# Kernel tuning notes

Measured on AMD Instinct MI355X. Metric: run time of the kernel, lower is better.

## Reference

```python
import jax, jax.numpy as jnp
import numpy as np

B, T, IN, H, OUT = 1024, 2048, 16, 128, 1


def setup_inputs() -> dict:
    key = jax.random.key(0)
    ks = jax.random.split(key, 4)
    x = jax.random.normal(ks[0], (B, T, IN), dtype=jnp.float32)
    W_ih = jax.random.normal(ks[1], (4 * H, IN), dtype=jnp.float32) * (1.0 / np.sqrt(H))
    W_hh = jax.random.normal(ks[2], (4 * H, H), dtype=jnp.float32) * (1.0 / np.sqrt(H))
    b_ih = jnp.zeros((4 * H,), dtype=jnp.float32)
    b_hh = jnp.zeros((4 * H,), dtype=jnp.float32)
    # xavier_normal_ for fc.weight, zeros for bias
    fc_w = jax.random.normal(ks[3], (OUT, H), dtype=jnp.float32) * np.sqrt(2.0 / (H + OUT))
    fc_b = jnp.zeros((OUT,), dtype=jnp.float32)
    return {"x": x, "W_ih": W_ih, "W_hh": W_hh, "b_ih": b_ih,
            "b_hh": b_hh, "fc_w": fc_w, "fc_b": fc_b}


def reference(x, W_ih, W_hh, b_ih, b_hh, fc_w, fc_b):
    # SLSTM with reset_mechanism='none': mem == LSTM hidden h, syn == cell c;
    # spikes are discarded, so this is a plain LSTMCell recurrence + final Linear.
    b, t, _ = x.shape
    h = W_hh.shape[1]
    # Precompute input contribution to gates for all timesteps: (T, B, 4H)
    xg = jnp.einsum('bti,gi->tbg', x, W_ih) + (b_ih + b_hh)

    def step(carry, xg_t):
        h_t, c_t = carry
        gates = xg_t + h_t @ W_hh.T  # (B, 4H)
        i_g, f_g, g_g, o_g = jnp.split(gates, 4, axis=-1)
        c_new = jax.nn.sigmoid(f_g) * c_t + jax.nn.sigmoid(i_g) * jnp.tanh(g_g)
        h_new = jax.nn.sigmoid(o_g) * jnp.tanh(c_new)
        return (h_new, c_new), None

    h0 = jnp.zeros((b, h), dtype=x.dtype)
    c0 = jnp.zeros((b, h), dtype=x.dtype)
    (h_final, _), _ = jax.lax.scan(step, (h0, c0), xg)
    return h_final @ fc_w.T + fc_b  # fc(mem)
```

## Files before the change

### kernel.cpp

```cpp
#include <hip/hip_runtime.h>
#include <hip/hip_bf16.h>


#define T_LEN 2048
#define IN_DIM 16
#define CHUNK 32
#define NROWS 4

typedef __attribute__((ext_vector_type(4))) float f32x4;
typedef __attribute__((ext_vector_type(8))) short s16x8;

__device__ __forceinline__ short f2bf(float f) {
    union { float f; unsigned u; } v; v.f = f;
    unsigned r = v.u + 0x7fffu + ((v.u >> 16) & 1u);
    return (short)(r >> 16);
}
__device__ __forceinline__ unsigned pk_bf16(float a, float b) {
#if __has_builtin(__builtin_amdgcn_cvt_pk_bf16_f32)
    typedef __attribute__((ext_vector_type(2))) __bf16 bf16x2;
    bf16x2 r = __builtin_amdgcn_cvt_pk_bf16_f32(a, b);
    union { bf16x2 v; unsigned u; } c; c.v = r;
    return c.u;
#else
    return (unsigned)(unsigned short)f2bf(a) | ((unsigned)(unsigned short)f2bf(b) << 16);
#endif
}
__device__ __forceinline__ float pack4(float r0, float r1, float r2, float r3) {
    int d = __float_as_int(r0);
    d = __builtin_amdgcn_update_dpp(d, __float_as_int(r1), 0x124, 0xF, 0x2, false);
    d = __builtin_amdgcn_update_dpp(d, __float_as_int(r2), 0x128, 0xF, 0x4, false);
    d = __builtin_amdgcn_update_dpp(d, __float_as_int(r3), 0x12C, 0xF, 0x8, false);
    return __int_as_float(d);
}

__global__ __launch_bounds__(512, 2)
void slstm_persistent(const float* __restrict__ x,
                      const float* __restrict__ W_ih,
                      const float* __restrict__ W_hh,
                      const float* __restrict__ b_ih,
                      const float* __restrict__ b_hh,
                      const float* __restrict__ fc_w,
                      const float* __restrict__ fc_b,
                      float* __restrict__ out)
{
    __shared__ __align__(16) unsigned short h_frag[2][512];
    __shared__ __align__(16) unsigned short xlds[2][CHUNK][2][4][8];
    __shared__ float red[NROWS];

    const int tid  = threadIdx.x;
    const int lane = tid & 63;
    const int wv   = tid >> 6;
    const int c16  = lane & 15;
    const int quad = lane >> 4;
    const int b0   = blockIdx.x * NROWS;

    const float kNL2E = -1.44269504f;

    s16x8 wfrag[4][5];
    f32x4 biasC[4];
    #pragma unroll
    for (int g = 0; g < 4; ++g) {
        const float scale = (g == 2) ? (2.0f * kNL2E) : kNL2E;
        const int n = g * 128 + wv * 16 + c16;
        #pragma unroll
        for (int kf = 0; kf < 5; ++kf) {
            s16x8 fr;
            #pragma unroll
            for (int j = 0; j < 8; ++j) {
                const int k = kf * 32 + quad * 8 + j;
                float v;
                if (kf < 4) v = W_hh[n * 128 + k];
                else {
                    const int kk = k - 128;
                    v = (kk < IN_DIM) ? W_ih[n * IN_DIM + kk] : 0.0f;
                }
                fr[j] = f2bf(v * scale);
            }
            wfrag[g][kf] = fr;
        }
        #pragma unroll
        for (int r = 0; r < 4; ++r) {
            const int m = g * 128 + wv * 16 + quad * 4 + r;
            biasC[g][r] = (b_ih[m] + b_hh[m]) * scale;
        }
    }

    if (tid < 256) ((unsigned*)h_frag)[tid] = 0;

    const int e    = c16 >> 2;
    const int nb   = c16 & 3;
    const int col  = wv * 16 + quad * 4 + e;
    const int waddr = (col >> 5) * 128 + ((col >> 3) & 3) * 32 + nb * 8 + (col & 7);
    const int hoff = (c16 < 4) ? ((quad * 4 + c16) * 16) : 0;
    const bool xv = (quad < 2) && (c16 < 4);
    const int xoff  = xv ? (quad * 64 + c16 * 16) : 0;
    const int xmask = xv ? ~0 : 0;

    float c_st = 0.0f, h_ep = 0.0f;

    f32x4 xreg;
    {
        const int flat4 = tid * 4;
        const int b_loc = flat4 >> 9;
        const int rem   = flat4 & 511;
        const float* xr = x + (size_t)(b0 + b_loc) * (T_LEN * IN_DIM);
        f32x4 v4 = *(const f32x4*)(xr + rem);
        const int slot = rem >> 4, feat = rem & 15;
        unsigned* dst = (unsigned*)&xlds[0][slot][feat >> 3][b_loc][feat & 7];
        dst[0] = pk_bf16(v4[0], v4[1]);
        dst[1] = pk_bf16(v4[2], v4[3]);
        xreg = *(const f32x4*)(xr + CHUNK * IN_DIM + rem);
    }
    __syncthreads();

    f32x4 accA[4], accB[4];
    {
        s16x8 zx0 = *(const s16x8*)((const char*)xlds + (xoff & xmask));
        #pragma unroll
        for (int g = 0; g < 4; ++g)
            accA[g] = __builtin_amdgcn_mfma_f32_16x16x32_bf16(wfrag[g][4], zx0, biasC[g], 0, 0, 0);
    }

    int off_cur = 128 + xoff;

    auto step_impl = [&](const int RB, const int WB, f32x4 (&aci)[4], f32x4 (&aco)[4]) {
        const char* hb = (const char*)h_frag[RB];
        s16x8 zf[4];
        #pragma unroll
        for (int kf = 0; kf < 4; ++kf)
            zf[kf] = *(const s16x8*)(hb + hoff + kf * 256);
        s16x8 zxn = *(const s16x8*)((const char*)xlds + (off_cur & xmask));
        off_cur = (off_cur + 128) & 8191;

        #pragma unroll
        for (int kf = 0; kf < 4; ++kf) {
            aci[2] = __builtin_amdgcn_mfma_f32_16x16x32_bf16(wfrag[2][kf], zf[kf], aci[2], 0, 0, 0);
            aci[0] = __builtin_amdgcn_mfma_f32_16x16x32_bf16(wfrag[0][kf], zf[kf], aci[0], 0, 0, 0);
            aci[1] = __builtin_amdgcn_mfma_f32_16x16x32_bf16(wfrag[1][kf], zf[kf], aci[1], 0, 0, 0);
        }
        __builtin_amdgcn_sched_barrier(0);

        aci[3] = __builtin_amdgcn_mfma_f32_16x16x32_bf16(wfrag[3][0], zf[0], aci[3], 0, 0, 0);
        aci[3] = __builtin_amdgcn_mfma_f32_16x16x32_bf16(wfrag[3][1], zf[1], aci[3], 0, 0, 0);
        aci[3] = __builtin_amdgcn_mfma_f32_16x16x32_bf16(wfrag[3][2], zf[2], aci[3], 0, 0, 0);
        aci[3] = __builtin_amdgcn_mfma_f32_16x16x32_bf16(wfrag[3][3], zf[3], aci[3], 0, 0, 0);
        const float dg = pack4(aci[2][0], aci[2][1], aci[2][2], aci[2][3]);
        const float eg = __builtin_amdgcn_exp2f(dg);
        const float di = pack4(aci[0][0], aci[0][1], aci[0][2], aci[0][3]);
        const float ei = __builtin_amdgcn_exp2f(di);
        const float df = pack4(aci[1][0], aci[1][1], aci[1][2], aci[1][3]);
        const float ef = __builtin_amdgcn_exp2f(df);
        const float af  = 1.0f + ef;
        const float t1  = (1.0f + ei) * (1.0f + eg);
        const float num = fmaf(c_st, t1, (1.0f - eg) * af);
        const float den = af * t1;
        const float dojj = pack4(aci[3][0], aci[3][1], aci[3][2], aci[3][3]);
        const float eo  = __builtin_amdgcn_exp2f(dojj);
        const float p_o = 1.0f + eo;
        #pragma unroll
        for (int kq = 0; kq < 4; ++kq) {
            __builtin_amdgcn_sched_group_barrier(0x008, 1, 0);
            __builtin_amdgcn_sched_group_barrier(0x002, 6, 0);
        }
        __builtin_amdgcn_sched_barrier(0);

        aco[0] = __builtin_amdgcn_mfma_f32_16x16x32_bf16(wfrag[0][4], zxn, biasC[0], 0, 0, 0);
        aco[1] = __builtin_amdgcn_mfma_f32_16x16x32_bf16(wfrag[1][4], zxn, biasC[1], 0, 0, 0);
        const float cn = num * __builtin_amdgcn_rcpf(den);
        c_st = cn;
        const float ec = __builtin_amdgcn_exp2f(fminf(cn * (2.0f * kNL2E), 40.f));
        const float hn = (1.0f - ec) * __builtin_amdgcn_rcpf(p_o * (1.0f + ec));
        h_ep = hn;
        h_frag[WB][waddr] = (unsigned short)pk_bf16(hn, hn);
        aco[2] = __builtin_amdgcn_mfma_f32_16x16x32_bf16(wfrag[2][4], zxn, biasC[2], 0, 0, 0);
        aco[3] = __builtin_amdgcn_mfma_f32_16x16x32_bf16(wfrag[3][4], zxn, biasC[3], 0, 0, 0);
        __syncthreads();
    };

    for (int t = 0; t < T_LEN; t += 2) {
        step_impl(0, 1, accA, accB);

        const int iter  = (t >> 1) & 15;
        const int cbase = t & ~(CHUNK - 1);
        if (iter < 2) {
            if (cbase + CHUNK < T_LEN) {
                const int flat4 = tid * 4;
                const int b_loc = flat4 >> 9;
                const int rem   = flat4 & 511;
                const int slot = rem >> 4, feat = rem & 15;
                const int nb1 = ((cbase >> 5) + 1) & 1;
                unsigned* dst = (unsigned*)&xlds[nb1][slot][feat >> 3][b_loc][(feat & 7) + 2 * iter];
                dst[0] = pk_bf16(xreg[2 * iter], xreg[2 * iter + 1]);
            }
        } else if (iter == 8) {
            const int tnext = cbase + 2 * CHUNK;
            if (tnext < T_LEN) {
                const int flat4 = tid * 4;
                const int b_loc = flat4 >> 9;
                const int rem   = flat4 & 511;
                xreg = *(const f32x4*)(x + (size_t)(b0 + b_loc) * (T_LEN * IN_DIM)
                                         + (size_t)tnext * IN_DIM + rem);
            }
        }

        step_impl(1, 0, accB, accA);
    }

    float v = h_ep * fc_w[col];
    v += __shfl_xor(v, 4);
    v += __shfl_xor(v, 8);
    v += __shfl_xor(v, 16);
    v += __shfl_xor(v, 32);
    if (tid < NROWS) red[tid] = 0.0f;
    __syncthreads();
    if (lane < NROWS) atomicAdd(&red[nb], v);
    __syncthreads();
    if (tid < NROWS) out[b0 + tid] = red[tid] + fc_b[0];
}

extern "C" void kernel_launch(void* const* d_in, const int* in_sizes, int n_in,
                              void* d_out, int out_size, void* d_ws, size_t ws_size,
                              hipStream_t stream) {
    const float* x    = (const float*)d_in[0];
    const float* W_ih = (const float*)d_in[1];
    const float* W_hh = (const float*)d_in[2];
    const float* b_ih = (const float*)d_in[3];
    const float* b_hh = (const float*)d_in[4];
    const float* fc_w = (const float*)d_in[5];
    const float* fc_b = (const float*)d_in[6];
    float* out = (float*)d_out;

    slstm_persistent<<<256, 512, 0, stream>>>(x, W_ih, W_hh, b_ih, b_hh, fc_w, fc_b, out);
}
```

Before: 1.210 ms.

## Rotate h buffers across four phases and hoist input-projection MFMAs per phase

Replaces the two-buffer ping-pong of hidden-state fragments with a five-slot buffer rotated over four timestep phases, and changes the DPP pack to a per-phase rotated lane selection. Each step now issues a single input-projection MFMA for one gate instead of four, with x staged in a new interleaved LDS layout that packs four timesteps per 16x32 fragment. The aim is to cut the per-step MFMA count and LDS reads on the serial recurrence critical path. It adds more LDS, extra zero-initialization and more complex index bookkeeping, with a risk of subtle ordering errors across phases.

Result: faster. 1.058 ms (-12.6%).

```diff
diff --git a/kernel.cpp b/kernel.cpp
--- a/kernel.cpp
+++ b/kernel.cpp
@@ -1,5 +1,6 @@
 #include <hip/hip_runtime.h>
 #include <hip/hip_bf16.h>
+#include <type_traits>
 
 
 #define T_LEN 2048
@@ -25,11 +26,12 @@
     return (unsigned)(unsigned short)f2bf(a) | ((unsigned)(unsigned short)f2bf(b) << 16);
 #endif
 }
-__device__ __forceinline__ float pack4(float r0, float r1, float r2, float r3) {
-    int d = __float_as_int(r0);
-    d = __builtin_amdgcn_update_dpp(d, __float_as_int(r1), 0x124, 0xF, 0x2, false);
-    d = __builtin_amdgcn_update_dpp(d, __float_as_int(r2), 0x128, 0xF, 0x4, false);
-    d = __builtin_amdgcn_update_dpp(d, __float_as_int(r3), 0x12C, 0xF, 0x8, false);
+template<int P>
+__device__ __forceinline__ float pack4p(const f32x4& a) {
+    int d = __float_as_int(a[P]);
+    d = __builtin_amdgcn_update_dpp(d, __float_as_int(a[(P + 1) & 3]), 0x124, 0xF, 1 << ((P + 1) & 3), false);
+    d = __builtin_amdgcn_update_dpp(d, __float_as_int(a[(P + 2) & 3]), 0x128, 0xF, 1 << ((P + 2) & 3), false);
+    d = __builtin_amdgcn_update_dpp(d, __float_as_int(a[(P + 3) & 3]), 0x12C, 0xF, 1 << ((P + 3) & 3), false);
     return __int_as_float(d);
 }
 
@@ -43,8 +45,8 @@
                       const float* __restrict__ fc_b,
                       float* __restrict__ out)
 {
-    __shared__ __align__(16) unsigned short h_frag[2][512];
-    __shared__ __align__(16) unsigned short xlds[2][CHUNK][2][4][8];
+    __shared__ __align__(16) unsigned short h_frag[5][512];
+    __shared__ __align__(16) unsigned short xq[8192];
     __shared__ float red[NROWS];
 
     const int tid  = threadIdx.x;
@@ -85,16 +87,25 @@
         }
     }
 
-    if (tid < 256) ((unsigned*)h_frag)[tid] = 0;
+    {
+        unsigned* hz = (unsigned*)h_frag;
+        hz[tid] = 0; hz[tid + 512] = 0;
+        if (tid < 256) hz[tid + 1024] = 0;
+        unsigned* xz = (unsigned*)xq;
+        #pragma unroll
+        for (int i = 0; i < 8; ++i) xz[tid + i * 512] = 0;
+    }
+    __syncthreads();
 
     const int e    = c16 >> 2;
     const int nb   = c16 & 3;
     const int col  = wv * 16 + quad * 4 + e;
     const int waddr = (col >> 5) * 128 + ((col >> 3) & 3) * 32 + nb * 8 + (col & 7);
-    const int hoff = (c16 < 4) ? ((quad * 4 + c16) * 16) : 0;
-    const bool xv = (quad < 2) && (c16 < 4);
-    const int xoff  = xv ? (quad * 64 + c16 * 16) : 0;
-    const int xmask = xv ? ~0 : 0;
+    int hoffP[4];
+    #pragma unroll
+    for (int q = 0; q < 4; ++q)
+        hoffP[q] = (((c16 >> 2) == q) ? ((q + 3) & 3) : 4) * 1024
+                 + (quad * 4 + (c16 & 3)) * 16;
 
     float c_st = 0.0f, h_ep = 0.0f;
 
@@ -105,56 +116,57 @@
         const int rem   = flat4 & 511;
         const float* xr = x + (size_t)(b0 + b_loc) * (T_LEN * IN_DIM);
         f32x4 v4 = *(const f32x4*)(xr + rem);
-        const int slot = rem >> 4, feat = rem & 15;
-        unsigned* dst = (unsigned*)&xlds[0][slot][feat >> 3][b_loc][feat & 7];
+        const int slot = rem >> 4, f = rem & 15;
+        const int qs = slot >> 2, s = slot & 3;
+        unsigned* dst = (unsigned*)&xq[qs * 512 + (f >> 3) * 128 + (4 * s + b_loc) * 8 + (f & 7)];
         dst[0] = pk_bf16(v4[0], v4[1]);
         dst[1] = pk_bf16(v4[2], v4[3]);
         xreg = *(const f32x4*)(xr + CHUNK * IN_DIM + rem);
     }
     __syncthreads();
 
+    const char* xb = (const char*)xq;
+    s16x8 zx4r = *(const s16x8*)(xb + lane * 16);
     f32x4 accA[4], accB[4];
-    {
-        s16x8 zx0 = *(const s16x8*)((const char*)xlds + (xoff & xmask));
-        #pragma unroll
-        for (int g = 0; g < 4; ++g)
-            accA[g] = __builtin_amdgcn_mfma_f32_16x16x32_bf16(wfrag[g][4], zx0, biasC[g], 0, 0, 0);
-    }
-
-    int off_cur = 128 + xoff;
-
-    auto step_impl = [&](const int RB, const int WB, f32x4 (&aci)[4], f32x4 (&aco)[4]) {
-        const char* hb = (const char*)h_frag[RB];
+    #pragma unroll
+    for (int g = 0; g < 4; ++g)
+        accA[g] = __builtin_amdgcn_mfma_f32_16x16x32_bf16(wfrag[g][4], zx4r, biasC[g], 0, 0, 0);
+    zx4r = *(const s16x8*)(xb + 1024 + lane * 16);
+    int xqoff = 2 * 1024 + lane * 16;
+
+    const char* hb = (const char*)h_frag;
+    unsigned short* hw = (unsigned short*)h_frag;
+
+    auto phaseF = [&](auto Pc, f32x4 (&acc)[4], f32x4 (&accn)[4]) {
+        constexpr int P = decltype(Pc)::value;
         s16x8 zf[4];
         #pragma unroll
         for (int kf = 0; kf < 4; ++kf)
-            zf[kf] = *(const s16x8*)(hb + hoff + kf * 256);
-        s16x8 zxn = *(const s16x8*)((const char*)xlds + (off_cur & xmask));
-        off_cur = (off_cur + 128) & 8191;
+            zf[kf] = *(const s16x8*)(hb + hoffP[P] + kf * 256);
 
         #pragma unroll
         for (int kf = 0; kf < 4; ++kf) {
-            aci[2] = __builtin_amdgcn_mfma_f32_16x16x32_bf16(wfrag[2][kf], zf[kf], aci[2], 0, 0, 0);
-            aci[0] = __builtin_amdgcn_mfma_f32_16x16x32_bf16(wfrag[0][kf], zf[kf], aci[0], 0, 0, 0);
-            aci[1] = __builtin_amdgcn_mfma_f32_16x16x32_bf16(wfrag[1][kf], zf[kf], aci[1], 0, 0, 0);
+            acc[2] = __builtin_amdgcn_mfma_f32_16x16x32_bf16(wfrag[2][kf], zf[kf], acc[2], 0, 0, 0);
+            acc[0] = __builtin_amdgcn_mfma_f32_16x16x32_bf16(wfrag[0][kf], zf[kf], acc[0], 0, 0, 0);
+            acc[1] = __builtin_amdgcn_mfma_f32_16x16x32_bf16(wfrag[1][kf], zf[kf], acc[1], 0, 0, 0);
         }
         __builtin_amdgcn_sched_barrier(0);
 
-        aci[3] = __builtin_amdgcn_mfma_f32_16x16x32_bf16(wfrag[3][0], zf[0], aci[3], 0, 0, 0);
-        aci[3] = __builtin_amdgcn_mfma_f32_16x16x32_bf16(wfrag[3][1], zf[1], aci[3], 0, 0, 0);
-        aci[3] = __builtin_amdgcn_mfma_f32_16x16x32_bf16(wfrag[3][2], zf[2], aci[3], 0, 0, 0);
-        aci[3] = __builtin_amdgcn_mfma_f32_16x16x32_bf16(wfrag[3][3], zf[3], aci[3], 0, 0, 0);
-        const float dg = pack4(aci[2][0], aci[2][1], aci[2][2], aci[2][3]);
+        acc[3] = __builtin_amdgcn_mfma_f32_16x16x32_bf16(wfrag[3][0], zf[0], acc[3], 0, 0, 0);
+        acc[3] = __builtin_amdgcn_mfma_f32_16x16x32_bf16(wfrag[3][1], zf[1], acc[3], 0, 0, 0);
+        acc[3] = __builtin_amdgcn_mfma_f32_16x16x32_bf16(wfrag[3][2], zf[2], acc[3], 0, 0, 0);
+        acc[3] = __builtin_amdgcn_mfma_f32_16x16x32_bf16(wfrag[3][3], zf[3], acc[3], 0, 0, 0);
+        const float dg = pack4p<P>(acc[2]);
         const float eg = __builtin_amdgcn_exp2f(dg);
-        const float di = pack4(aci[0][0], aci[0][1], aci[0][2], aci[0][3]);
+        const float di = pack4p<P>(acc[0]);
         const float ei = __builtin_amdgcn_exp2f(di);
-        const float df = pack4(aci[1][0], aci[1][1], aci[1][2], aci[1][3]);
+        const float df = pack4p<P>(acc[1]);
         const float ef = __builtin_amdgcn_exp2f(df);
         const float af  = 1.0f + ef;
         const float t1  = (1.0f + ei) * (1.0f + eg);
         const float num = fmaf(c_st, t1, (1.0f - eg) * af);
         const float den = af * t1;
-        const float dojj = pack4(aci[3][0], aci[3][1], aci[3][2], aci[3][3]);
+        const float dojj = pack4p<P>(acc[3]);
         const float eo  = __builtin_amdgcn_exp2f(dojj);
         const float p_o = 1.0f + eo;
         #pragma unroll
@@ -164,36 +176,37 @@
         }
         __builtin_amdgcn_sched_barrier(0);
 
-        aco[0] = __builtin_amdgcn_mfma_f32_16x16x32_bf16(wfrag[0][4], zxn, biasC[0], 0, 0, 0);
-        aco[1] = __builtin_amdgcn_mfma_f32_16x16x32_bf16(wfrag[1][4], zxn, biasC[1], 0, 0, 0);
+        accn[P] = __builtin_amdgcn_mfma_f32_16x16x32_bf16(wfrag[P][4], zx4r, biasC[P], 0, 0, 0);
         const float cn = num * __builtin_amdgcn_rcpf(den);
         c_st = cn;
         const float ec = __builtin_amdgcn_exp2f(fminf(cn * (2.0f * kNL2E), 40.f));
         const float hn = (1.0f - ec) * __builtin_amdgcn_rcpf(p_o * (1.0f + ec));
         h_ep = hn;
-        h_frag[WB][waddr] = (unsigned short)pk_bf16(hn, hn);
-        aco[2] = __builtin_amdgcn_mfma_f32_16x16x32_bf16(wfrag[2][4], zxn, biasC[2], 0, 0, 0);
-        aco[3] = __builtin_amdgcn_mfma_f32_16x16x32_bf16(wfrag[3][4], zxn, biasC[3], 0, 0, 0);
+        hw[P * 512 + waddr] = (unsigned short)pk_bf16(hn, hn);
+        if constexpr (P == 3) {
+            zx4r = *(const s16x8*)(xb + xqoff);
+            xqoff = (xqoff + 1024) & 16383;
+        }
         __syncthreads();
     };
 
-    for (int t = 0; t < T_LEN; t += 2) {
-        step_impl(0, 1, accA, accB);
-
-        const int iter  = (t >> 1) & 15;
-        const int cbase = t & ~(CHUNK - 1);
-        if (iter < 2) {
-            if (cbase + CHUNK < T_LEN) {
+    auto maint = [&](int Q) {
+        const int qi = Q & 7;
+        const int chunkI = Q >> 3;
+        if (qi < 2) {
+            if (chunkI < (T_LEN / CHUNK) - 1) {
                 const int flat4 = tid * 4;
                 const int b_loc = flat4 >> 9;
                 const int rem   = flat4 & 511;
-                const int slot = rem >> 4, feat = rem & 15;
-                const int nb1 = ((cbase >> 5) + 1) & 1;
-                unsigned* dst = (unsigned*)&xlds[nb1][slot][feat >> 3][b_loc][(feat & 7) + 2 * iter];
-                dst[0] = pk_bf16(xreg[2 * iter], xreg[2 * iter + 1]);
+                const int slot = rem >> 4, f = rem & 15;
+                const int qs = slot >> 2, s = slot & 3;
+                const int nb1 = (chunkI + 1) & 1;
+                const int k0 = f + 2 * qi;
+                unsigned* dst = (unsigned*)&xq[nb1 * 4096 + qs * 512 + (k0 >> 3) * 128 + (4 * s + b_loc) * 8 + (k0 & 7)];
+                dst[0] = pk_bf16(xreg[2 * qi], xreg[2 * qi + 1]);
             }
-        } else if (iter == 8) {
-            const int tnext = cbase + 2 * CHUNK;
+        } else if (qi == 4) {
+            const int tnext = (chunkI + 2) * CHUNK;
             if (tnext < T_LEN) {
                 const int flat4 = tid * 4;
                 const int b_loc = flat4 >> 9;
@@ -202,8 +215,19 @@
                                          + (size_t)tnext * IN_DIM + rem);
             }
         }
-
-        step_impl(1, 0, accB, accA);
+    };
+
+    for (int Q = 0; Q < T_LEN / 4; Q += 2) {
+        phaseF(std::integral_constant<int, 0>{}, accA, accB);
+        maint(Q);
+        phaseF(std::integral_constant<int, 1>{}, accA, accB);
+        phaseF(std::integral_constant<int, 2>{}, accA, accB);
+        phaseF(std::integral_constant<int, 3>{}, accA, accB);
+        phaseF(std::integral_constant<int, 0>{}, accB, accA);
+        maint(Q + 1);
+        phaseF(std::integral_constant<int, 1>{}, accB, accA);
+        phaseF(std::integral_constant<int, 2>{}, accB, accA);
+        phaseF(std::integral_constant<int, 3>{}, accB, accA);
     }
 
     float v = h_ep * fc_w[col];
```
